# Performance work log

Measured on AMD Instinct MI355X. Metric: run time of the kernel, lower is better.

The kernel has to match this reference:

```python
import jax, jax.numpy as jnp
import numpy as np
from functools import partial

H = 2048   # image height
W = 2048   # image width
FC_IN = 1024
FC_OUT = 10


def setup_inputs() -> dict:
    key = jax.random.key(0)
    ks = jax.random.split(key, 7)
    x = jax.random.normal(ks[0], (1, H, W), dtype=jnp.float32)
    # Conv2d(1,1,1): scalar weight + bias
    w_in = jax.random.normal(ks[1], (1, 1, 1, 1), dtype=jnp.float32)
    b_in = jax.random.normal(ks[2], (1,), dtype=jnp.float32) * 0.1
    # Conv1d(1,1,2,padding=1): 2-tap kernel + bias
    w_state = jax.random.normal(ks[3], (1, 1, 2), dtype=jnp.float32) * 0.5
    b_state = jax.random.normal(ks[4], (1,), dtype=jnp.float32) * 0.1
    # Linear(1024, 10)
    fc_w = jax.random.normal(ks[5], (FC_OUT, FC_IN), dtype=jnp.float32) * (1.0 / np.sqrt(FC_IN))
    fc_b = jax.random.normal(ks[6], (FC_OUT,), dtype=jnp.float32) * 0.1
    return {"x": x, "w_in": w_in, "b_in": b_in, "w_state": w_state,
            "b_state": b_state, "fc_w": fc_w, "fc_b": fc_b}


def reference(x, w_in, b_in, w_state, b_state, fc_w, fc_b):
    img = x[0]                      # [H, W]
    h_dim, w_dim = img.shape
    w_skew = w_dim + h_dim - 1      # skewed image width

    # --- skew: row r shifted right by r, zero-filled elsewhere ---
    rows = jnp.arange(h_dim)[:, None]          # [H,1]
    cols = jnp.arange(w_dim)[None, :] + rows   # [H,W] destination columns
    skewed = jnp.zeros((h_dim, w_skew), dtype=img.dtype).at[rows, cols].set(img)

    # --- 1x1 input convolution: scalar affine ---
    input_matrix = skewed * w_in[0, 0, 0, 0] + b_in[0]   # [H, Wskew]

    k0 = w_state[0, 0, 0]
    k1 = w_state[0, 0, 1]
    bs = b_state[0]

    # --- sequential column scan: h_c = tanh(k0*shift(h) + k1*h + bs + inp_c) ---
    def step(h, inp_col):
        shifted = jnp.concatenate([jnp.zeros((1,), h.dtype), h[:-1]])
        a = jnp.tanh(k0 * shifted + k1 * h + bs + inp_col)
        return a, a

    h0 = jnp.zeros((h_dim,), dtype=img.dtype)
    _, acts = jax.lax.scan(step, h0, input_matrix.T)     # acts: [Wskew, H]

    # --- unskew: unskewed[r, c] = acts[r + c, r] ---
    c_idx = jnp.arange(w_dim)[None, :]                   # [1, W]
    unskewed = acts[rows + c_idx, rows]                  # [H, W]

    flat = unskewed.reshape(-1, FC_IN)                   # [H*W/1024, 1024]
    return flat @ fc_w.T + fc_b                          # [H*W/1024, 10]
```

## Files before the change

kernel.cpp:

```cpp
#include <hip/hip_runtime.h>

#define HH 2048
#define WW 2048
#define WSK 4095
#define WSKP 4096
#define BLKS 8
#define NW  4
#define NT  (NW * 64)
#define KCH 32
#define NCH (WSKP / KCH)
#define FC_IN 1024
#define FC_OUT 10
#define NFLAT ((HH * WW) / FC_IN)

__device__ __forceinline__ float tanh_pre(float xs) {
  float e = __builtin_amdgcn_exp2f(xs);
  float r = __builtin_amdgcn_rcpf(e + 1.0f);
  return __builtin_fmaf(-2.0f, r, 1.0f);
}

__device__ __forceinline__ float wave_shr1(float src, float old) {
  int r = __builtin_amdgcn_update_dpp(
      __builtin_bit_cast(int, old), __builtin_bit_cast(int, src),
      0x138 , 0xF, 0xF, false);
  return __builtin_bit_cast(float, r);
}

__global__ __launch_bounds__(256) void skew_kernel(
    const float* __restrict__ img, const float* __restrict__ w_in,
    const float* __restrict__ b_in, const float* __restrict__ b_state,
    float* __restrict__ inp) {
  const float S = 2.88539008177792681472f;
  const float ws = w_in[0] * S;
  const float Cs = (b_in[0] + b_state[0]) * S;
  int gid = blockIdx.x * 256 + threadIdx.x;
  int r = gid & (HH - 1);
  int c = gid >> 11;
  int idx = c - r;
  float v = Cs;
  if ((unsigned)idx < (unsigned)WW) v = fmaf(ws, img[(size_t)r * WW + idx], Cs);
  inp[gid] = v;
}

__global__ __launch_bounds__(NT) void scan_kernel(
    const float* __restrict__ w_state, const float* __restrict__ inp,
    float* __restrict__ acts, unsigned* __restrict__ flags) {
  const int t = threadIdx.x;
  const int wv = t >> 6;
  const int lane = t & 63;
  const int blk = blockIdx.x;
  const int r = blk * NT + t;

  const float S = 2.88539008177792681472f;
  const float k0s = w_state[0] * S;
  const float k1s = w_state[1] * S;

  __shared__ float ring[2][NW][KCH];

  float h = 0.0f;
  const float* colp_in = inp + r;
  float* colp_out = acts + r;

  float pf[KCH];
  #pragma unroll
  for (int d = 0; d < KCH; ++d) pf[d] = colp_in[(size_t)d * HH];

  const unsigned* upflag = flags + (blk - 1) * NCH;
  unsigned* myflag = flags + blk * NCH;
  const float* uprow = acts + (blk * NT - 1);

  for (int e = 0; e < NCH + NW - 1; ++e) {
    const int ch = e - wv;
    if (0 <= ch && ch < NCH) {
      const int c0 = ch * KCH;

      float bvec;
      if (wv == 0) {
        bvec = 0.0f;
        if (blk > 0) {
          const unsigned want = (unsigned)(ch + 1);
          while (__hip_atomic_load(upflag + ch, __ATOMIC_ACQUIRE,
                                   __HIP_MEMORY_SCOPE_AGENT) != want)
            __builtin_amdgcn_s_sleep(1);
          int cl = c0 + lane - 1;
          if (lane < KCH && cl >= 0) bvec = uprow[(size_t)cl * HH];
        }
      } else {
        bvec = ring[(e & 1) ^ 1][wv - 1][lane & (KCH - 1)];
      }
      if (lane == 63) ring[e & 1][wv][0] = h;

      const int cb = (ch + 1 < NCH ? ch + 1 : ch) * KCH;

      #pragma unroll
      for (int cc = 0; cc < KCH; ++cc) {
        float cur = pf[cc];
        pf[cc] = colp_in[(size_t)(cb + cc) * HH];

        float pv = __builtin_bit_cast(float,
            __builtin_amdgcn_readlane(__builtin_bit_cast(int, bvec), cc));
        float prev = wave_shr1(h, pv);

        h = tanh_pre(fmaf(k0s, prev, fmaf(k1s, h, cur)));

        if (lane == 63 && cc + 1 < KCH) ring[e & 1][wv][cc + 1] = h;
        colp_out[(size_t)(c0 + cc) * HH] = h;
      }

      if (wv == NW - 1 && lane == 63)
        __hip_atomic_store(myflag + ch, (unsigned)(ch + 1), __ATOMIC_RELEASE,
                           __HIP_MEMORY_SCOPE_AGENT);
    }
    asm volatile("s_waitcnt lgkmcnt(0)\n\ts_barrier" ::: "memory");
  }
}

__global__ __launch_bounds__(64) void fc_kernel(
    const float* __restrict__ acts, const float* __restrict__ fc_w,
    const float* __restrict__ fc_b, float* __restrict__ out) {
  const int i = blockIdx.x;
  const int lane = threadIdx.x;
  const int r = i >> 1;
  const int base = (i & 1) << 10;

  float acc[FC_OUT];
  #pragma unroll
  for (int j = 0; j < FC_OUT; ++j) acc[j] = 0.0f;

  for (int k = lane; k < FC_IN; k += 64) {
    float v = acts[(size_t)(r + base + k) * HH + r];
    #pragma unroll
    for (int j = 0; j < FC_OUT; ++j)
      acc[j] = fmaf(v, fc_w[j * FC_IN + k], acc[j]);
  }

  #pragma unroll
  for (int j = 0; j < FC_OUT; ++j) {
    #pragma unroll
    for (int off = 32; off > 0; off >>= 1)
      acc[j] += __shfl_down(acc[j], off);
  }

  if (lane == 0) {
    #pragma unroll
    for (int j = 0; j < FC_OUT; ++j)
      out[i * FC_OUT + j] = acc[j] + fc_b[j];
  }
}

extern "C" void kernel_launch(void* const* d_in, const int* in_sizes, int n_in,
                              void* d_out, int out_size, void* d_ws, size_t ws_size,
                              hipStream_t stream) {
  const float* x       = (const float*)d_in[0];
  const float* w_in    = (const float*)d_in[1];
  const float* b_in    = (const float*)d_in[2];
  const float* w_state = (const float*)d_in[3];
  const float* b_state = (const float*)d_in[4];
  const float* fc_w    = (const float*)d_in[5];
  const float* fc_b    = (const float*)d_in[6];
  float* out = (float*)d_out;
  float* buf = (float*)d_ws;

  unsigned* flags = (unsigned*)d_out;

  skew_kernel<<<(WSKP * HH) / 256, 256, 0, stream>>>(x, w_in, b_in, b_state, buf);
  scan_kernel<<<BLKS, NT, 0, stream>>>(w_state, buf, buf, flags);
  fc_kernel<<<NFLAT, 64, 0, stream>>>(buf, fc_w, fc_b, out);
}
```

Before: 554.2 us.

## Tile skew via LDS, reshape scan blocks, prefetch upstream boundary, coalesce FC reads

The skew kernel now stages 64x128 image tiles in shared memory so that both the reads and the column-major writes are coalesced. The scan uses 4 blocks of 8 waves instead of 8 blocks of 4, which shortens the inter-block flag chain. Wave 0 now waits on the upstream block's next chunk one step ahead, so the wait overlaps the current chunk's compute. Ring writes are made branchless through a dummy LDS slot, and the last block no longer publishes flags. The FC kernel is restructured so that each lane owns one row r and walks diagonals with coalesced reads across lanes, then reduces through LDS. The risk is a longer intra-block wave pipeline and many conditional FC iterations.

```diff
diff --git a/kernel.cpp b/kernel.cpp
--- a/kernel.cpp
+++ b/kernel.cpp
@@ -4,14 +4,13 @@
 #define WW 2048
 #define WSK 4095
 #define WSKP 4096
-#define BLKS 8
-#define NW  4
+#define BLKS 4
+#define NW  8
 #define NT  (NW * 64)
 #define KCH 32
 #define NCH (WSKP / KCH)
 #define FC_IN 1024
 #define FC_OUT 10
-#define NFLAT ((HH * WW) / FC_IN)
 
 __device__ __forceinline__ float tanh_pre(float xs) {
   float e = __builtin_amdgcn_exp2f(xs);
@@ -26,20 +25,41 @@
   return __builtin_bit_cast(float, r);
 }
 
+#define TS_PAD 130
 __global__ __launch_bounds__(256) void skew_kernel(
     const float* __restrict__ img, const float* __restrict__ w_in,
     const float* __restrict__ b_in, const float* __restrict__ b_state,
     float* __restrict__ inp) {
+  __shared__ float tile[64 * TS_PAD];
   const float S = 2.88539008177792681472f;
   const float ws = w_in[0] * S;
   const float Cs = (b_in[0] + b_state[0]) * S;
-  int gid = blockIdx.x * 256 + threadIdx.x;
-  int r = gid & (HH - 1);
-  int c = gid >> 11;
-  int idx = c - r;
-  float v = Cs;
-  if ((unsigned)idx < (unsigned)WW) v = fmaf(ws, img[(size_t)r * WW + idx], Cs);
-  inp[gid] = v;
+  const int t = threadIdx.x;
+  const int lane = t & 63;
+  const int g = t >> 6;
+  const int c0 = (blockIdx.x & 63) * 64;
+  const int r0 = (blockIdx.x >> 6) * 64;
+  const int cin0 = c0 - r0 - 63;
+
+  for (int i = g; i < 64; i += 4) {
+    const float* rowp = img + (size_t)(r0 + i) * WW;
+    int ca = cin0 + lane;
+    int cb = cin0 + 64 + lane;
+    int cca = ca < 0 ? 0 : (ca > WW - 1 ? WW - 1 : ca);
+    int ccb = cb < 0 ? 0 : (cb > WW - 1 ? WW - 1 : cb);
+    tile[i * TS_PAD + lane] = rowp[cca];
+    tile[i * TS_PAD + 64 + lane] = rowp[ccb];
+  }
+  __syncthreads();
+
+  for (int cc = g; cc < 64; cc += 4) {
+    int c = c0 + cc;
+    int cin = c - r0 - lane;
+    int q = cc + 63 - lane;
+    float raw = tile[lane * TS_PAD + q];
+    float v = ((unsigned)cin < (unsigned)WW) ? fmaf(ws, raw, Cs) : Cs;
+    inp[(size_t)c * HH + r0 + lane] = v;
+  }
 }
 
 __global__ __launch_bounds__(NT) void scan_kernel(
@@ -56,6 +76,7 @@
   const float k1s = w_state[1] * S;
 
   __shared__ float ring[2][NW][KCH];
+  __shared__ float dump[NW][KCH];
 
   float h = 0.0f;
   const float* colp_in = inp + r;
@@ -65,30 +86,38 @@
   #pragma unroll
   for (int d = 0; d < KCH; ++d) pf[d] = colp_in[(size_t)d * HH];
 
-  const unsigned* upflag = flags + (blk - 1) * NCH;
+  unsigned* upflag = flags + (blk - 1) * NCH;
   unsigned* myflag = flags + blk * NCH;
   const float* uprow = acts + (blk * NT - 1);
+
+  float bcur = 0.0f, bnext = 0.0f;
+  if (wv == 0 && blk > 0) {
+    while (__hip_atomic_load(upflag + 0, __ATOMIC_ACQUIRE,
+                             __HIP_MEMORY_SCOPE_AGENT) != 1u)
+      __builtin_amdgcn_s_sleep(1);
+    int cl = lane - 1;
+    if (lane < KCH && cl >= 0) bcur = uprow[(size_t)cl * HH];
+  }
 
   for (int e = 0; e < NCH + NW - 1; ++e) {
     const int ch = e - wv;
     if (0 <= ch && ch < NCH) {
       const int c0 = ch * KCH;
 
+      if (wv == 0 && blk > 0 && ch + 1 < NCH) {
+        const unsigned want = (unsigned)(ch + 2);
+        while (__hip_atomic_load(upflag + (ch + 1), __ATOMIC_ACQUIRE,
+                                 __HIP_MEMORY_SCOPE_AGENT) != want)
+          __builtin_amdgcn_s_sleep(1);
+        bnext = 0.0f;
+        if (lane < KCH) bnext = uprow[(size_t)(c0 + KCH + lane - 1) * HH];
+      }
+
       float bvec;
-      if (wv == 0) {
-        bvec = 0.0f;
-        if (blk > 0) {
-          const unsigned want = (unsigned)(ch + 1);
-          while (__hip_atomic_load(upflag + ch, __ATOMIC_ACQUIRE,
-                                   __HIP_MEMORY_SCOPE_AGENT) != want)
-            __builtin_amdgcn_s_sleep(1);
-          int cl = c0 + lane - 1;
-          if (lane < KCH && cl >= 0) bvec = uprow[(size_t)cl * HH];
-        }
-      } else {
-        bvec = ring[(e & 1) ^ 1][wv - 1][lane & (KCH - 1)];
-      }
-      if (lane == 63) ring[e & 1][wv][0] = h;
+      if (wv == 0) bvec = bcur;
+      else bvec = ring[(e & 1) ^ 1][wv - 1][lane & (KCH - 1)];
+
+      { float* a = (lane == 63) ? &ring[e & 1][wv][0] : &dump[wv][0]; *a = h; }
 
       const int cb = (ch + 1 < NCH ? ch + 1 : ch) * KCH;
 
@@ -103,48 +132,70 @@
 
         h = tanh_pre(fmaf(k0s, prev, fmaf(k1s, h, cur)));
 
-        if (lane == 63 && cc + 1 < KCH) ring[e & 1][wv][cc + 1] = h;
+        float* a = (lane == 63 && cc + 1 < KCH) ? &ring[e & 1][wv][cc + 1]
+                                                : &dump[wv][cc];
+        *a = h;
+
         colp_out[(size_t)(c0 + cc) * HH] = h;
       }
 
-      if (wv == NW - 1 && lane == 63)
+      if (wv == NW - 1 && blk < BLKS - 1 && lane == 63)
         __hip_atomic_store(myflag + ch, (unsigned)(ch + 1), __ATOMIC_RELEASE,
                            __HIP_MEMORY_SCOPE_AGENT);
+      if (wv == 0) bcur = bnext;
     }
     asm volatile("s_waitcnt lgkmcnt(0)\n\ts_barrier" ::: "memory");
   }
 }
 
-__global__ __launch_bounds__(64) void fc_kernel(
+__global__ __launch_bounds__(256) void fc_kernel(
     const float* __restrict__ acts, const float* __restrict__ fc_w,
     const float* __restrict__ fc_b, float* __restrict__ out) {
-  const int i = blockIdx.x;
-  const int lane = threadIdx.x;
-  const int r = i >> 1;
-  const int base = (i & 1) << 10;
-
-  float acc[FC_OUT];
+  __shared__ float red[4][64][2 * FC_OUT];
+  const int t = threadIdx.x;
+  const int lane = t & 63;
+  const int g = t >> 6;
+  const int r0 = blockIdx.x * 64;
+  const int r = r0 + lane;
+
+  float acc0[FC_OUT], acc1[FC_OUT];
   #pragma unroll
-  for (int j = 0; j < FC_OUT; ++j) acc[j] = 0.0f;
-
-  for (int k = lane; k < FC_IN; k += 64) {
-    float v = acts[(size_t)(r + base + k) * HH + r];
-    #pragma unroll
-    for (int j = 0; j < FC_OUT; ++j)
-      acc[j] = fmaf(v, fc_w[j * FC_IN + k], acc[j]);
+  for (int j = 0; j < FC_OUT; ++j) { acc0[j] = 0.0f; acc1[j] = 0.0f; }
+
+  #pragma unroll 4
+  for (int m = 0; m < 528; ++m) {
+    int d = r0 + g + 4 * m;
+    float a = acts[(size_t)d * HH + r];
+    int c = d - r;
+    if ((unsigned)c < 1024u) {
+      #pragma unroll
+      for (int j = 0; j < FC_OUT; ++j)
+        acc0[j] = fmaf(a, fc_w[j * FC_IN + c], acc0[j]);
+    } else if ((unsigned)c < 2048u) {
+      int k = c - 1024;
+      #pragma unroll
+      for (int j = 0; j < FC_OUT; ++j)
+        acc1[j] = fmaf(a, fc_w[j * FC_IN + k], acc1[j]);
+    }
   }
 
   #pragma unroll
   for (int j = 0; j < FC_OUT; ++j) {
+    red[g][lane][j] = acc0[j];
+    red[g][lane][FC_OUT + j] = acc1[j];
+  }
+  __syncthreads();
+
+  if (g == 0) {
     #pragma unroll
-    for (int off = 32; off > 0; off >>= 1)
-      acc[j] += __shfl_down(acc[j], off);
-  }
-
-  if (lane == 0) {
-    #pragma unroll
-    for (int j = 0; j < FC_OUT; ++j)
-      out[i * FC_OUT + j] = acc[j] + fc_b[j];
+    for (int j = 0; j < FC_OUT; ++j) {
+      float s0 = red[0][lane][j] + red[1][lane][j] +
+                 red[2][lane][j] + red[3][lane][j];
+      float s1 = red[0][lane][FC_OUT + j] + red[1][lane][FC_OUT + j] +
+                 red[2][lane][FC_OUT + j] + red[3][lane][FC_OUT + j];
+      out[(size_t)(2 * r) * FC_OUT + j] = s0 + fc_b[j];
+      out[(size_t)(2 * r + 1) * FC_OUT + j] = s1 + fc_b[j];
+    }
   }
 }
 
@@ -163,7 +214,7 @@
 
   unsigned* flags = (unsigned*)d_out;
 
-  skew_kernel<<<(WSKP * HH) / 256, 256, 0, stream>>>(x, w_in, b_in, b_state, buf);
+  skew_kernel<<<64 * 32, 256, 0, stream>>>(x, w_in, b_in, b_state, buf);
   scan_kernel<<<BLKS, NT, 0, stream>>>(w_state, buf, buf, flags);
-  fc_kernel<<<NFLAT, 64, 0, stream>>>(buf, fc_w, fc_b, out);
-}
+  fc_kernel<<<HH / 64, 256, 0, stream>>>(buf, fc_w, fc_b, out);
+}
```

Result: slower. 758.6 us (+36.9%).
